# Kernel tuning notes

Measured on AMD Instinct MI355X. Metric: run time of the kernel, lower is better.

## Reference

```python
import jax, jax.numpy as jnp
import numpy as np

HID = 256; HEADS = 8; HD = HID // HEADS; GROUPS = 8; CPG = HID // GROUPS
DIMS = [64, 128, 256, 512]; SIZES = [56, 28, 14, 7]; B = 8


def _linear(x, W, b):
    # torch nn.Linear convention: W is [out, in]
    return jnp.einsum('...i,oi->...o', x, W) + b


def _conv1x1(x, W, b):
    return jnp.einsum('bchw,oc->bohw', x, W) + b[None, :, None, None]


def setup_inputs() -> dict:
    key = jax.random.key(0)
    keys = iter(jax.random.split(key, 64))
    def nrm(shape, s=0.02):
        return jax.random.normal(next(keys), shape, dtype=jnp.float32) * s
    inp = {}
    for i, (d, sz) in enumerate(zip(DIMS, SIZES)):
        inp[f'f{i}'] = jax.random.normal(next(keys), (B, d, sz, sz), dtype=jnp.float32)
        inp[f'Wp{i}'] = nrm((HID, d)); inp[f'bp{i}'] = jnp.zeros((HID,), jnp.float32)
    for n, shp in [('Wq', (HID, HID)), ('Wk', (HID, HID)), ('Wv', (HID, HID)), ('Wo', (HID, HID)),
                   ('Wg1', (HID, 2 * HID)), ('Wg2', (HID, HID)), ('Wcp', (HID, HID)),
                   ('Wkg1', (2 * HID, HID)), ('Wkg2', (GROUPS * 9, 2 * HID)),
                   ('Wit', (HID, HID)), ('Wot', (HID, HID))]:
        inp[n] = nrm(shp)
    for n, dim in [('bq', HID), ('bk', HID), ('bv', HID), ('bo', HID), ('bg1', HID), ('bg2', HID),
                   ('bcp', HID), ('bkg1', 2 * HID), ('bkg2', GROUPS * 9), ('bit', HID), ('bot', HID)]:
        inp[n] = jnp.zeros((dim,), jnp.float32)
    inp['gamma'] = jnp.ones((HID,), jnp.float32)
    inp['beta'] = jnp.zeros((HID,), jnp.float32)
    return inp


def reference(f0, f1, f2, f3, Wp0, bp0, Wp1, bp1, Wp2, bp2, Wp3, bp3,
              Wq, bq, Wk, bk, Wv, bv, Wo, bo, Wg1, bg1, Wg2, bg2,
              Wcp, bcp, Wkg1, bkg1, Wkg2, bkg2, Wit, bit, Wot, bot, gamma, beta):
    feats = [f0, f1, f2, f3]
    Wps = [Wp0, Wp1, Wp2, Wp3]; bps = [bp0, bp1, bp2, bp3]
    b = f0.shape[0]
    # ---- ACSA: 1x1 projections to hidden_dim, flatten spatial to tokens ----
    proj = [_conv1x1(f, W, bb) for f, W, bb in zip(feats, Wps, bps)]  # [B,HID,H,W]
    flat = [p.reshape(b, HID, -1).transpose(0, 2, 1) for p in proj]   # [B,S,HID]
    scale = 1.0 / jnp.sqrt(jnp.float32(HD))
    enhanced = []
    for i, xi in enumerate(flat):
        q = _linear(xi, Wq, bq).reshape(b, -1, HEADS, HD).transpose(0, 2, 1, 3)  # [B,H,Si,d]
        e = xi
        for j, xj in enumerate(flat):
            if i == j:
                continue
            k = _linear(xj, Wk, bk).reshape(b, -1, HEADS, HD).transpose(0, 2, 1, 3)
            v = _linear(xj, Wv, bv).reshape(b, -1, HEADS, HD).transpose(0, 2, 1, 3)
            attn = jax.nn.softmax(jnp.einsum('bhqd,bhkd->bhqk', q, k) * scale, axis=-1)
            ctx = jnp.einsum('bhqk,bhkd->bhqd', attn, v).transpose(0, 2, 1, 3).reshape(b, -1, HID)
            ctx = _linear(ctx, Wo, bo)
            gate = jax.nn.sigmoid(_linear(jax.nn.relu(_linear(jnp.concatenate([e, ctx], -1), Wg1, bg1)), Wg2, bg2))
            e = e + gate * ctx
        enhanced.append(e.transpose(0, 2, 1).reshape(b, HID, proj[i].shape[2], proj[i].shape[3]))
    # ---- CECM per scale: dynamic per-sample grouped 3x3 conv ----
    outs = []
    for x in enhanced:
        H, W = x.shape[2], x.shape[3]
        ctx = jax.nn.relu(_linear(x.mean((2, 3)), Wcp, bcp))                       # [B,HID]
        kern = _linear(jax.nn.relu(_linear(ctx, Wkg1, bkg1)), Wkg2, bkg2)          # [B,G*9]
        kern = kern.reshape(b, GROUPS, 3, 3)
        xt = _conv1x1(x, Wit, bit)                                                 # [B,HID,H,W]
        # per-(sample,group) kernel shared across channels within group -> depthwise conv
        kern_rep = jnp.broadcast_to(kern[:, :, None], (b, GROUPS, CPG, 3, 3)).reshape(b * HID, 1, 3, 3)
        y = jax.lax.conv_general_dilated(
            xt.reshape(1, b * HID, H, W), kern_rep, (1, 1), ((1, 1), (1, 1)),
            dimension_numbers=('NCHW', 'OIHW', 'NCHW'), feature_group_count=b * HID
        ).reshape(b, HID, H, W)
        y = _conv1x1(y, Wot, bot)
        # BatchNorm2d (training-mode batch statistics, biased var, eps=1e-5)
        mu = y.mean((0, 2, 3)); var = y.var((0, 2, 3))
        y = (y - mu[None, :, None, None]) * jax.lax.rsqrt(var + 1e-5)[None, :, None, None]
        y = y * gamma[None, :, None, None] + beta[None, :, None, None]
        outs.append((xt + y).reshape(b, HID, -1))
    # concat scales along flattened-spatial axis -> [B, HID, 3136+784+196+49]
    return jnp.concatenate(outs, axis=-1)
```

## Files before the change

### kernel.cpp

```cpp
#include <hip/hip_runtime.h>
#include <hip/hip_bf16.h>
#include <cstddef>

#define NB 8
#define HIDC 256
#define NHEAD 8
#define HDIM 32
#define TTOK 33320
#define STOT 4165
#define VTP 33440
#define QKVS 768
#define QSC2 0.2550348757f
#define BN1_CH 128

static const int H_SZ[4]   = {56, 28, 14, 7};
static const int S_SZ[4]   = {3136, 784, 196, 49};
static const int D_IN[4]   = {64, 128, 256, 512};
static const int BOFF[4]   = {0, 25088, 31360, 32928};
static const int SKPAD_H[4]= {3136, 784, 200, 56};
static const int VWOFF_H[4]= {0, 25088, 31360, 32960};

__constant__ int DC_S[4]     = {3136, 784, 196, 49};
__constant__ int DC_HW[4]    = {56, 28, 14, 7};
__constant__ int DC_BOFF[4]  = {0, 25088, 31360, 32928};
__constant__ int DC_GOFF[4]  = {0, 3136, 3920, 4116};
__constant__ int DC_FOS[4]   = {0, 49, 62, 66};

__constant__ int FP_SQ[12]   = {784,196,49,3136,196,49,3136,784,49,3136,784,196};
__constant__ int FP_SK[12]   = {3136,3136,3136,784,784,784,196,196,196,49,49,49};
__constant__ int FP_QOFF[12] = {25088,31360,32928,0,31360,32928,0,25088,32928,0,25088,31360};
__constant__ int FP_KOFF[12] = {0,0,0,25088,25088,25088,31360,31360,31360,32928,32928,32928};
__constant__ int FP_VOFF[12] = {0,0,0,25088,25088,25088,31360,31360,31360,32960,32960,32960};
__constant__ int FP_SKP[12]  = {3136,3136,3136,784,784,784,200,200,200,56,56,56};
__constant__ int FP_R[12]    = {0,0,0,0,1,1,1,1,2,2,2,2};
__constant__ int FP_SB0[13]  = {0,13,17,18,31,32,33,46,50,51,64,68,69};

typedef short bf16s;
typedef bf16s bf16x8 __attribute__((ext_vector_type(8)));
typedef float f32x4 __attribute__((ext_vector_type(4)));

static __device__ inline bf16s f2b(float f) {
    return (bf16s)((__float_as_uint(f) + 0x8000u) >> 16);
}
static __device__ inline float b2f(bf16s s) {
    return __uint_as_float(((unsigned)(unsigned short)s) << 16);
}
static __device__ inline unsigned cvtpk(float a, float b) {
    unsigned r;
    asm("v_cvt_pk_bf16_f32 %0, %1, %2" : "=v"(r) : "v"(a), "v"(b));
    return r;
}
static __device__ inline float ex2(float x) {
#if __has_builtin(__builtin_amdgcn_exp2f)
    return __builtin_amdgcn_exp2f(x);
#else
    return exp2f(x);
#endif
}
#define MFMA16(a, b, c) __builtin_amdgcn_mfma_f32_16x16x32_bf16(a, b, c, 0, 0, 0)
#define ZERO4 ((f32x4){0.f, 0.f, 0.f, 0.f})

struct CvtArgs {
    const float* src[15];
    void* dst[15];
    int n[15];
    int mode[15];
    int K[15];
};
__global__ __launch_bounds__(256) void cvt_all(CvtArgs a, int total) {
    int idx = blockIdx.x * 256 + threadIdx.x;
    if (idx >= total) return;
    int seg = 0, off = idx;
    while (off >= a.n[seg]) { off -= a.n[seg]; seg++; }
    float v = a.src[seg][off];
    int m = a.mode[seg];
    if (m == 1 || m == 3) v *= QSC2;
    if (m <= 1) {
        int K = a.K[seg];
        int kz = __builtin_ctz(K);
        int n = off >> kz, k = off & (K - 1);
        int c64 = n >> 6, nt = (n >> 4) & 3, l15 = n & 15;
        int k32 = k >> 5, q = (k >> 3) & 3, j = k & 7;
        int dst = (((c64 * (K >> 5) + k32) * 4 + nt) << 9) + l15 * 32 + q * 8 + j;
        ((bf16s*)a.dst[seg])[dst] = f2b(v);
    } else {
        ((float*)a.dst[seg])[off] = v;
    }
}

__global__ __launch_bounds__(256) void transpose_f2(const float* __restrict__ f,
                                                    bf16s* __restrict__ A, int D, int S) {
    __shared__ float t[32][33];
    int s0 = blockIdx.x * 32, d0 = blockIdx.y * 32, b = blockIdx.z;
    int sl = threadIdx.x & 31, dl = threadIdx.x >> 5;
    #pragma unroll
    for (int dd = 0; dd < 32; dd += 8) {
        int s = s0 + sl;
        t[dl + dd][sl] = (s < S) ? f[((size_t)(b * D + d0 + dl + dd)) * S + s] : 0.f;
    }
    __syncthreads();
    int dc = threadIdx.x & 31, sg = threadIdx.x >> 5;
    #pragma unroll
    for (int ss = 0; ss < 32; ss += 8) {
        int s = s0 + sg + ss;
        if (s < S) A[((size_t)(b * S + s)) * D + d0 + dc] = f2b(t[dc][sg + ss]);
    }
}

template <int EPI>
__global__ __launch_bounds__(256) void gemm3(
    const bf16s* __restrict__ A, const bf16s* __restrict__ A2,
    const bf16s* __restrict__ W, const float* __restrict__ bias,
    float* __restrict__ Cf, bf16s* __restrict__ Cb, const bf16s* __restrict__ Gaux,
    int M, int N, int K, int K1)
{
    int tid = threadIdx.x, lane = tid & 63, wave = tid >> 6;
    int l15 = lane & 15, quad = lane >> 4;
    int row0 = blockIdx.y * 64 + (wave >> 1) * 32;
    int col0 = blockIdx.x * 128 + (wave & 1) * 64;
    int K2 = K - K1;
    int nk = K >> 5;
    int c64 = (blockIdx.x << 1) + (wave & 1);
    const bf16s* wbase = W + (size_t)c64 * ((size_t)nk << 11) + l15 * 32 + quad * 8;
    int ra[2];
    #pragma unroll
    for (int mt = 0; mt < 2; mt++) ra[mt] = min(row0 + mt * 16 + l15, M - 1);

    f32x4 acc[2][4];
    #pragma unroll
    for (int i = 0; i < 2; i++)
        #pragma unroll
        for (int j = 0; j < 4; j++) acc[i][j] = ZERO4;

    bf16x8 aA[2], wA[4], aB[2], wB[4];

    auto loadA = [&](bf16x8* af, int k32) {
        int kk = (k32 << 5) + quad * 8;
        if (kk < K1) {
            #pragma unroll
            for (int mt = 0; mt < 2; mt++)
                af[mt] = *(const bf16x8*)(A + (size_t)ra[mt] * K1 + kk);
        } else {
            int k2 = kk - K1;
            #pragma unroll
            for (int mt = 0; mt < 2; mt++)
                af[mt] = *(const bf16x8*)(A2 + (size_t)ra[mt] * K2 + k2);
        }
    };
    auto loadW = [&](bf16x8* wf, int k32) {
        const bf16s* p = wbase + ((size_t)k32 << 11);
        #pragma unroll
        for (int nt = 0; nt < 4; nt++)
            wf[nt] = *(const bf16x8*)(p + nt * 512);
    };

    loadA(aA, 0); loadW(wA, 0);
    for (int k32 = 0; k32 < nk; k32 += 2) {
        loadA(aB, k32 + 1); loadW(wB, k32 + 1);
        #pragma unroll
        for (int mt = 0; mt < 2; mt++)
            #pragma unroll
            for (int nt = 0; nt < 4; nt++)
                acc[mt][nt] = MFMA16(aA[mt], wA[nt], acc[mt][nt]);
        if (k32 + 2 < nk) { loadA(aA, k32 + 2); loadW(wA, k32 + 2); }
        #pragma unroll
        for (int mt = 0; mt < 2; mt++)
            #pragma unroll
            for (int nt = 0; nt < 4; nt++)
                acc[mt][nt] = MFMA16(aB[mt], wB[nt], acc[mt][nt]);
    }

    #pragma unroll
    for (int mt = 0; mt < 2; mt++) {
        int rowb = row0 + mt * 16 + quad * 4;
        #pragma unroll
        for (int nt = 0; nt < 4; nt++) {
            int col = col0 + nt * 16 + l15;
            float bv = bias ? bias[col] : 0.f;
            #pragma unroll
            for (int r = 0; r < 4; r++) {
                int row = rowb + r;
                if (row >= M) continue;
                size_t off = (size_t)row * N + col;
                float v = acc[mt][nt][r] + bv;
                if (EPI == 0) {
                    Cb[off] = f2b(v);
                } else if (EPI == 1) {
                    Cf[off] = v; Cb[off] = f2b(v);
                } else if (EPI == 2) {
                    float g = 1.f / (1.f + __expf(-v));
                    float e = Cf[off] + g * b2f(Gaux[off]);
                    Cf[off] = e; Cb[off] = f2b(e);
                } else if (EPI == 3) {
                    Cb[off] = f2b(fmaxf(v, 0.f));
                } else {
                    Cf[off] = v;
                }
            }
        }
    }
}

__global__ __launch_bounds__(256) void transpose_v(const bf16s* __restrict__ vsrc,
                                                   bf16s* __restrict__ vdst,
                                                   int Mtok, int Sk, int SkPad, int voff, int VS) {
    __shared__ bf16s t[64][72];
    int t0 = blockIdx.x * 64, d0 = blockIdx.y * 64;
    int tid = threadIdx.x;
    int lr = tid >> 2, lc = (tid & 3) * 16;
    if (t0 + lr < Mtok) {
        bf16x8 v0 = *(const bf16x8*)(vsrc + (size_t)(t0 + lr) * VS + d0 + lc);
        bf16x8 v1 = *(const bf16x8*)(vsrc + (size_t)(t0 + lr) * VS + d0 + lc + 8);
        *(bf16x8*)&t[lr][lc] = v0;
        *(bf16x8*)&t[lr][lc + 8] = v1;
    }
    __syncthreads();
    int dr = tid >> 2, tc = (tid & 3) * 16;
    #pragma unroll
    for (int u = 0; u < 16; u++) {
        int tok = t0 + tc + u;
        if (tok >= Mtok) break;
        int bidx = tok / Sk, s = tok - bidx * Sk;
        vdst[(size_t)(d0 + dr) * VTP + voff + bidx * SkPad + s] = t[tc + u][dr];
    }
}

__global__ __launch_bounds__(256) void flash8(const bf16s* __restrict__ qkv,
                                              const bf16s* __restrict__ vtb,
                                              bf16s* __restrict__ ctxall)
{
    __shared__ bf16s L[4][64 * 40];
    __shared__ float CMB[3][16][64];
    __shared__ float CLS[3][4][64];
    int bx = blockIdx.x;
    int sbg = bx >> 6, hb = bx & 63;
    int h = hb & 7, b = hb >> 3;
    int p = 0;
    while (sbg >= FP_SB0[p + 1]) p++;
    int wave = threadIdx.x >> 6, lane = threadIdx.x & 63;
    int l15 = lane & 15, quad = lane >> 4;
    int Sq = FP_SQ[p], Sk = FP_SK[p];
    bool ksp = (p < 3);
    int qrow0 = ksp ? (sbg - FP_SB0[p]) * 64
                    : ((sbg - FP_SB0[p]) * 4 + wave) * 64;
    if (qrow0 >= Sq) return;
    int k0 = ksp ? wave * 784 : 0;
    int klim = ksp ? 784 : Sk;
    int qoff = FP_QOFF[p], koff = FP_KOFF[p];
    int voff = FP_VOFF[p], skp = FP_SKP[p];
    bf16s* ctxr = ctxall + (size_t)FP_R[p] * TTOK * HIDC;

    const bf16s* qrow = qkv + (size_t)(qoff + b * Sq) * QKVS + h * HDIM + quad * 8;
    bf16x8 qf[4];
    #pragma unroll
    for (int qi = 0; qi < 4; qi++)
        qf[qi] = *(const bf16x8*)(qrow + (size_t)min(qrow0 + qi * 16 + l15, Sq - 1) * QKVS);

    const bf16s* kp0 = qkv + 256 + (size_t)(koff + b * Sk + k0 + l15) * QKVS + h * HDIM + quad * 8;
    const bf16s* kp16 = kp0 + (size_t)16 * QKVS;
    const bf16s* vp0 = vtb + (size_t)(h * HDIM + l15) * VTP + voff + b * skp + k0 + quad * 8;
    const bf16s* vp16 = vp0 + (size_t)16 * VTP;
    bf16s* Lw = L[wave];

    f32x4 a0[4], a1[4];
    float ls[4];
    #pragma unroll
    for (int qi = 0; qi < 4; qi++) { a0[qi] = ZERO4; a1[qi] = ZERO4; ls[qi] = 0.f; }
    int niter = (klim + 31) >> 5;

    bf16x8 kA0, kA1, vA0, vA1, kB0, kB1, vB0, vB1;

    auto loadKV = [&](bf16x8& kf0, bf16x8& kf1, bf16x8& vf0, bf16x8& vf1, int t) {
        size_t kb = (size_t)(t << 5) * QKVS;
        kf0 = *(const bf16x8*)(kp0 + kb);
        kf1 = *(const bf16x8*)(kp16 + kb);
        vf0 = *(const bf16x8*)(vp0 + (t << 5));
        vf1 = *(const bf16x8*)(vp16 + (t << 5));
    };
    auto compute = [&](bf16x8 kf0, bf16x8 kf1, bf16x8 vf0, bf16x8 vf1, int t) {
        int kt = t << 5;
        f32x4 s0[4], s1[4];
        #pragma unroll
        for (int qi = 0; qi < 4; qi++) {
            s0[qi] = MFMA16(kf0, qf[qi], ZERO4);
            s1[qi] = MFMA16(kf1, qf[qi], ZERO4);
        }
        float p0[4][4], p1[4][4];
        #pragma unroll
        for (int qi = 0; qi < 4; qi++)
            #pragma unroll
            for (int r = 0; r < 4; r++) {
                p0[qi][r] = ex2(s0[qi][r]);
                p1[qi][r] = ex2(s1[qi][r]);
            }
        if (kt + 32 > klim) {
            int lim0 = klim - kt - quad * 4, lim1 = lim0 - 16;
            #pragma unroll
            for (int qi = 0; qi < 4; qi++)
                #pragma unroll
                for (int r = 0; r < 4; r++) {
                    if (r >= lim0) p0[qi][r] = 0.f;
                    if (r >= lim1) p1[qi][r] = 0.f;
                }
        }
        #pragma unroll
        for (int qi = 0; qi < 4; qi++) {
            #pragma unroll
            for (int r = 0; r < 4; r++) ls[qi] += p0[qi][r] + p1[qi][r];
            *(uint2*)&Lw[(qi * 16 + l15) * 40 + quad * 4] =
                make_uint2(cvtpk(p0[qi][0], p0[qi][1]), cvtpk(p0[qi][2], p0[qi][3]));
            *(uint2*)&Lw[(qi * 16 + l15) * 40 + 16 + quad * 4] =
                make_uint2(cvtpk(p1[qi][0], p1[qi][1]), cvtpk(p1[qi][2], p1[qi][3]));
        }
        #pragma unroll
        for (int qi = 0; qi < 4; qi++) {
            bf16x8 pb = *(const bf16x8*)&Lw[(qi * 16 + l15) * 40 + quad * 8];
            a0[qi] = MFMA16(vf0, pb, a0[qi]);
            a1[qi] = MFMA16(vf1, pb, a1[qi]);
        }
    };

    loadKV(kA0, kA1, vA0, vA1, 0);
    for (int t = 0; t < niter; t += 2) {
        if (t + 1 < niter) loadKV(kB0, kB1, vB0, vB1, t + 1);
        compute(kA0, kA1, vA0, vA1, t);
        if (t + 2 < niter) loadKV(kA0, kA1, vA0, vA1, t + 2);
        if (t + 1 < niter) compute(kB0, kB1, vB0, vB1, t + 1);
    }

    if (ksp) {
        if (wave > 0) {
            #pragma unroll
            for (int qi = 0; qi < 4; qi++) {
                #pragma unroll
                for (int r = 0; r < 4; r++) CMB[wave - 1][qi * 4 + r][lane] = a0[qi][r];
                CLS[wave - 1][qi][lane] = ls[qi];
            }
        }
        __syncthreads();
        if (wave == 0) {
            #pragma unroll
            for (int w = 0; w < 3; w++)
                #pragma unroll
                for (int qi = 0; qi < 4; qi++) {
                    #pragma unroll
                    for (int r = 0; r < 4; r++) a0[qi][r] += CMB[w][qi * 4 + r][lane];
                    ls[qi] += CLS[w][qi][lane];
                }
        }
        __syncthreads();
        if (wave > 0) {
            #pragma unroll
            for (int qi = 0; qi < 4; qi++)
                #pragma unroll
                for (int r = 0; r < 4; r++) CMB[wave - 1][qi * 4 + r][lane] = a1[qi][r];
        }
        __syncthreads();
        if (wave > 0) return;
        #pragma unroll
        for (int w = 0; w < 3; w++)
            #pragma unroll
            for (int qi = 0; qi < 4; qi++)
                #pragma unroll
                for (int r = 0; r < 4; r++) a1[qi][r] += CMB[w][qi * 4 + r][lane];
    }

    #pragma unroll
    for (int qi = 0; qi < 4; qi++) {
        float l = ls[qi];
        l += __shfl_xor(l, 16); l += __shfl_xor(l, 32);
        float inv = 1.f / l;
        if (qrow0 + qi * 16 + l15 < Sq) {
            size_t o = (size_t)(qoff + b * Sq + qrow0 + qi * 16 + l15) * HIDC + h * HDIM;
            *(uint2*)(ctxr + o + quad * 4) =
                make_uint2(cvtpk(a0[qi][0] * inv, a0[qi][1] * inv),
                           cvtpk(a0[qi][2] * inv, a0[qi][3] * inv));
            *(uint2*)(ctxr + o + 16 + quad * 4) =
                make_uint2(cvtpk(a1[qi][0] * inv, a1[qi][1] * inv),
                           cvtpk(a1[qi][2] * inv, a1[qi][3] * inv));
        }
    }
}

__global__ __launch_bounds__(256) void pool2(const bf16s* __restrict__ xb,
                                             float* __restrict__ partial) {
    int chunk = blockIdx.x, b = blockIdx.y, i = blockIdx.z;
    int c = threadIdx.x;
    int S = DC_S[i];
    int len = (S + 31) / 32;
    int s0 = chunk * len, s1 = min(S, s0 + len);
    float acc = 0.f;
    const bf16s* base = xb + (size_t)(DC_BOFF[i] + b * S) * HIDC + c;
    for (int s = s0; s < s1; s++) acc += b2f(base[(size_t)s * HIDC]);
    partial[(size_t)((i * NB + b) * 32 + chunk) * HIDC + c] = acc;
}

__global__ __launch_bounds__(256) void kgen2(
    const float* __restrict__ partial,
    const float* __restrict__ Wcp, const float* __restrict__ bcp,
    const float* __restrict__ Wkg1, const float* __restrict__ bkg1,
    const float* __restrict__ Wkg2, const float* __restrict__ bkg2,
    float* __restrict__ kern)
{
    __shared__ float pl[256], cv[256], h1[512];
    int b = blockIdx.x, i = blockIdx.y, t = threadIdx.x;
    float invS = 1.f / (float)DC_S[i];
    const float* pb = partial + (size_t)((i * NB + b) * 32) * HIDC;
    float s = 0.f;
    for (int jc = 0; jc < 32; jc++) s += pb[(size_t)jc * HIDC + t];
    pl[t] = s * invS;
    __syncthreads();
    float a = bcp[t];
    for (int k = 0; k < 256; k++) a += Wcp[t * 256 + k] * pl[k];
    cv[t] = fmaxf(a, 0.f);
    __syncthreads();
    for (int r = t; r < 512; r += 256) {
        float a2 = bkg1[r];
        for (int k = 0; k < 256; k++) a2 += Wkg1[r * 256 + k] * cv[k];
        h1[r] = fmaxf(a2, 0.f);
    }
    __syncthreads();
    if (t < 72) {
        float a3 = bkg2[t];
        for (int k = 0; k < 512; k++) a3 += Wkg2[t * 512 + k] * h1[k];
        kern[(i * NB + b) * 72 + t] = a3;
    }
}

__global__ __launch_bounds__(256) void dwconv2(const bf16s* __restrict__ xtb,
                                               const float* __restrict__ kern,
                                               bf16s* __restrict__ y) {
    int tok = blockIdx.x;
    int i = (tok >= DC_BOFF[1]) + (tok >= DC_BOFF[2]) + (tok >= DC_BOFF[3]);
    int S = DC_S[i], W = DC_HW[i];
    int local = tok - DC_BOFF[i];
    int b = local / S, s = local - b * S;
    int hh = s / W, ww = s - hh * W;
    int c = threadIdx.x;
    const float* kb = kern + (i * NB + b) * 72 + (c >> 5) * 9;
    const bf16s* xbase = xtb + (size_t)(DC_BOFF[i] + b * S) * HIDC + c;
    float acc = 0.f;
    #pragma unroll
    for (int ky = 0; ky < 3; ky++) {
        int hy = hh + ky - 1;
        if (hy < 0 || hy >= W) continue;
        #pragma unroll
        for (int kx = 0; kx < 3; kx++) {
            int wx = ww + kx - 1;
            if (wx < 0 || wx >= W) continue;
            acc += kb[ky * 3 + kx] * b2f(xbase[(size_t)(hy * W + wx) * HIDC]);
        }
    }
    y[(size_t)tok * HIDC + c] = f2b(acc);
}

__global__ __launch_bounds__(256) void bn1(const float* __restrict__ yo,
                                           float* __restrict__ bnp) {
    __shared__ float red[4][64][8];
    int chunk = blockIdx.x, i = blockIdx.y, t = threadIdx.x;
    int rg = t >> 6, cq = (t & 63) * 4;
    int Nrows = NB * DC_S[i];
    const float* base = yo + (size_t)DC_BOFF[i] * HIDC + cq;
    f32x4 s = ZERO4, ss = ZERO4;
    for (int r = chunk * 4 + rg; r < Nrows; r += BN1_CH * 4) {
        f32x4 v = *(const f32x4*)(base + (size_t)r * HIDC);
        s += v; ss += v * v;
    }
    #pragma unroll
    for (int j = 0; j < 4; j++) { red[rg][t & 63][j] = s[j]; red[rg][t & 63][4 + j] = ss[j]; }
    __syncthreads();
    if (t < 64) {
        #pragma unroll
        for (int j = 0; j < 4; j++) {
            float a = red[0][t][j] + red[1][t][j] + red[2][t][j] + red[3][t][j];
            float b = red[0][t][4 + j] + red[1][t][4 + j] + red[2][t][4 + j] + red[3][t][4 + j];
            bnp[(size_t)(i * BN1_CH + chunk) * 512 + t * 4 + j] = a;
            bnp[(size_t)(i * BN1_CH + chunk) * 512 + 256 + t * 4 + j] = b;
        }
    }
}
__global__ __launch_bounds__(256) void bn2(const float* __restrict__ bnp,
                                           float* __restrict__ stat) {
    int i = blockIdx.x, c = threadIdx.x;
    float s = 0.f, ss = 0.f;
    for (int ch = 0; ch < BN1_CH; ch++) {
        s += bnp[(size_t)(i * BN1_CH + ch) * 512 + c];
        ss += bnp[(size_t)(i * BN1_CH + ch) * 512 + 256 + c];
    }
    float inv = 1.f / (float)(NB * DC_S[i]);
    float mu = s * inv;
    float var = fmaxf(ss * inv - mu * mu, 0.f);
    stat[i * 512 + c] = mu;
    stat[i * 512 + 256 + c] = rsqrtf(var + 1e-5f);
}

__global__ __launch_bounds__(256) void final2(const bf16s* __restrict__ xtb,
                                              const float* __restrict__ yo,
                                              const float* __restrict__ stat,
                                              const float* __restrict__ gamma,
                                              const float* __restrict__ beta,
                                              float* __restrict__ out) {
    __shared__ float tile[64][65];
    int bx = blockIdx.x;
    int i = (bx >= DC_FOS[1]) + (bx >= DC_FOS[2]) + (bx >= DC_FOS[3]);
    int S = DC_S[i];
    int s0 = (bx - DC_FOS[i]) * 64;
    int cstrip = blockIdx.y, b = blockIdx.z;
    int g = threadIdx.x >> 6, sl = threadIdx.x & 63;
    {
        int c = cstrip * 64 + sl;
        float mu = stat[i * 512 + c], rstd = stat[i * 512 + 256 + c];
        float ga = gamma[c], be = beta[c];
        size_t rbase = (size_t)(DC_BOFF[i] + b * S) * HIDC + c;
        #pragma unroll
        for (int u = 0; u < 16; u++) {
            int s = s0 + g * 16 + u;
            if (s < S) {
                size_t r = rbase + (size_t)s * HIDC;
                tile[g * 16 + u][sl] = b2f(xtb[r]) + (yo[r] - mu) * rstd * ga + be;
            }
        }
    }
    __syncthreads();
    {
        int s = s0 + sl;
        if (s < S) {
            #pragma unroll
            for (int cs = 0; cs < 16; cs++) {
                int cl = g * 16 + cs;
                out[((size_t)(b * HIDC + cstrip * 64 + cl)) * STOT + DC_GOFF[i] + s] = tile[sl][cl];
            }
        }
    }
}

static inline void gemm_launch(hipStream_t st, const bf16s* A, const bf16s* A2,
                               const bf16s* W, const float* bias,
                               float* Cf, bf16s* Cb, const bf16s* Gaux,
                               int M, int N, int K, int K1, int epi) {
    dim3 grid(N / 128, (M + 63) / 64), blk(256);
    switch (epi) {
        case 0: gemm3<0><<<grid, blk, 0, st>>>(A, A2, W, bias, Cf, Cb, Gaux, M, N, K, K1); break;
        case 1: gemm3<1><<<grid, blk, 0, st>>>(A, A2, W, bias, Cf, Cb, Gaux, M, N, K, K1); break;
        case 2: gemm3<2><<<grid, blk, 0, st>>>(A, A2, W, bias, Cf, Cb, Gaux, M, N, K, K1); break;
        case 3: gemm3<3><<<grid, blk, 0, st>>>(A, A2, W, bias, Cf, Cb, Gaux, M, N, K, K1); break;
        default: gemm3<4><<<grid, blk, 0, st>>>(A, A2, W, bias, Cf, Cb, Gaux, M, N, K, K1); break;
    }
}

extern "C" void kernel_launch(void* const* d_in, const int* in_sizes, int n_in,
                              void* d_out, int out_size, void* d_ws, size_t ws_size,
                              hipStream_t stream) {
    typedef const float* fp;
    fp f[4]  = {(fp)d_in[0], (fp)d_in[3], (fp)d_in[6], (fp)d_in[9]};
    fp Wp[4] = {(fp)d_in[1], (fp)d_in[4], (fp)d_in[7], (fp)d_in[10]};
    fp bp[4] = {(fp)d_in[2], (fp)d_in[5], (fp)d_in[8], (fp)d_in[11]};
    fp Wq = (fp)d_in[12], Wk = (fp)d_in[13], Wv = (fp)d_in[14], Wo = (fp)d_in[15];
    fp Wg1 = (fp)d_in[16], Wg2 = (fp)d_in[17], Wcp = (fp)d_in[18];
    fp Wkg1 = (fp)d_in[19], Wkg2 = (fp)d_in[20], Wit = (fp)d_in[21], Wot = (fp)d_in[22];
    fp bq = (fp)d_in[23], bk = (fp)d_in[24], bv = (fp)d_in[25], bo = (fp)d_in[26];
    fp bg1 = (fp)d_in[27], bg2 = (fp)d_in[28], bcp = (fp)d_in[29];
    fp bkg1 = (fp)d_in[30], bkg2 = (fp)d_in[31], bit = (fp)d_in[32], bot = (fp)d_in[33];
    fp gamma = (fp)d_in[34], beta = (fp)d_in[35];
    float* out = (float*)d_out;

    const size_t NT = (size_t)TTOK * HIDC;

    float* x     = (float*)d_ws;
    bf16s* xb    = (bf16s*)(x + NT);
    bf16s* qkvb  = xb + NT;
    bf16s* vtb   = qkvb + (size_t)TTOK * QKVS;
    bf16s* ctxall= vtb + (size_t)HIDC * VTP;
    bf16s* ctxob = ctxall + 3 * NT;
    float* partial = (float*)(ctxob + 3 * NT);
    float* kern    = partial + 4 * NB * 32 * HIDC;
    float* bnp     = kern + 4 * NB * 72;
    float* bnstat  = bnp + 4 * 32 * 512;
    float* bqkv    = bnstat + 4 * 512;
    bf16s* wseg    = (bf16s*)(bqkv + 768);
    bf16s* atmp = ctxall;
    bf16s* hb   = ctxall;
    bf16s* xtb  = ctxall + NT;
    float* yo   = x;
    float* bnp2 = partial;

    bf16s* wpb[4]; size_t wo_ = 0;
    for (int i = 0; i < 4; i++) { wpb[i] = wseg + wo_; wo_ += (size_t)HIDC * D_IN[i]; }
    bf16s* wqkvb = wseg + wo_; wo_ += (size_t)QKVS * 256;
    bf16s* wob  = wseg + wo_; wo_ += 65536;
    bf16s* wg1b = wseg + wo_; wo_ += 131072;
    bf16s* wg2b = wseg + wo_; wo_ += 65536;
    bf16s* witb = wseg + wo_; wo_ += 65536;
    bf16s* wotb = wseg + wo_; wo_ += 65536;

    {
        CvtArgs ca;
        const float* srcs[15] = {Wp[0], Wp[1], Wp[2], Wp[3], Wq, Wk, Wv, Wo, Wg1, Wg2,
                                 Wit, Wot, bq, bk, bv};
        void* dsts[15] = {wpb[0], wpb[1], wpb[2], wpb[3], wqkvb, wqkvb + 65536,
                          wqkvb + 131072, wob, wg1b, wg2b, witb, wotb,
                          bqkv, bqkv + 256, bqkv + 512};
        int ns[15] = {16384, 32768, 65536, 131072, 65536, 65536, 65536, 65536, 131072,
                      65536, 65536, 65536, 256, 256, 256};
        int modes[15] = {0, 0, 0, 0, 1, 0, 0, 0, 0, 0, 0, 0, 3, 2, 2};
        int Ks[15] = {64, 128, 256, 512, 256, 256, 256, 256, 512, 256, 256, 256, 0, 0, 0};
        int total = 0;
        for (int k = 0; k < 15; k++) { ca.src[k] = srcs[k]; ca.dst[k] = dsts[k];
                                       ca.n[k] = ns[k]; ca.mode[k] = modes[k];
                                       ca.K[k] = Ks[k]; total += ns[k]; }
        cvt_all<<<dim3((total + 255) / 256), dim3(256), 0, stream>>>(ca, total);
    }
    hipMemsetAsync(vtb, 0, (size_t)HIDC * VTP * sizeof(bf16s), stream);

    for (int i = 0; i < 4; i++) {
        int S = S_SZ[i], D = D_IN[i], M = NB * S;
        transpose_f2<<<dim3((S + 31) / 32, D / 32, NB), dim3(256), 0, stream>>>(f[i], atmp, D, S);
        gemm_launch(stream, atmp, nullptr, wpb[i], bp[i],
                    x + (size_t)BOFF[i] * HIDC, xb + (size_t)BOFF[i] * HIDC, nullptr,
                    M, HIDC, D, D, 1);
    }

    gemm_launch(stream, xb, nullptr, wqkvb, bqkv, nullptr, qkvb, nullptr, TTOK, QKVS, 256, 256, 0);
    for (int j = 0; j < 4; j++) {
        int Mtok = NB * S_SZ[j];
        transpose_v<<<dim3((Mtok + 63) / 64, 4), dim3(256), 0, stream>>>(
            qkvb + 512 + (size_t)BOFF[j] * QKVS, vtb, Mtok, S_SZ[j], SKPAD_H[j], VWOFF_H[j], QKVS);
    }

    flash8<<<dim3(69 * 64), dim3(256), 0, stream>>>(qkvb, vtb, ctxall);
    gemm_launch(stream, ctxall, nullptr, wob, bo, nullptr, ctxob, nullptr, 3 * TTOK, HIDC, 256, 256, 0);
    for (int r = 0; r < 3; r++) {
        bf16s* cr = ctxob + (size_t)r * NT;
        gemm_launch(stream, xb, cr, wg1b, bg1, nullptr, hb, nullptr, TTOK, HIDC, 512, 256, 3);
        gemm_launch(stream, hb, nullptr, wg2b, bg2, x, xb, cr, TTOK, HIDC, 256, 256, 2);
    }

    pool2<<<dim3(32, NB, 4), dim3(256), 0, stream>>>(xb, partial);
    kgen2<<<dim3(NB, 4), dim3(256), 0, stream>>>(partial, Wcp, bcp, Wkg1, bkg1, Wkg2, bkg2, kern);
    gemm_launch(stream, xb, nullptr, witb, bit, nullptr, xtb, nullptr, TTOK, HIDC, 256, 256, 0);
    dwconv2<<<dim3(TTOK), dim3(256), 0, stream>>>(xtb, kern, hb);
    gemm_launch(stream, hb, nullptr, wotb, bot, yo, nullptr, nullptr, TTOK, HIDC, 256, 256, 4);
    bn1<<<dim3(BN1_CH, 4), dim3(256), 0, stream>>>(yo, bnp2);
    bn2<<<dim3(4), dim3(256), 0, stream>>>(bnp2, bnstat);
    final2<<<dim3(67, 4, NB), dim3(256), 0, stream>>>(xtb, yo, bnstat, gamma, beta, out);
}
```

Baseline: 999.4 us.

## Fuse three-round gating MLP chain into one kernel with LDS-resident activations

Replaces six GEMM launches (three rounds of gate-hidden relu GEMM and gate-output sigmoid GEMM) with one kernel per 32-row tile. The running fp32 state, its bf16 copy, context and hidden activations stay in registers and LDS across all three rounds. This removes the global round-trips of the hidden buffer and the repeated reads and writes of x/xb. Weights are now streamed from global memory per block without LDS staging, and the tile is smaller than the old 64x128 GEMM tile, so weight traffic per row rises and occupancy may drop.

Result: faster. 850.4 us (-14.9%).

```diff
diff --git a/kernel.cpp b/kernel.cpp
--- a/kernel.cpp
+++ b/kernel.cpp
@@ -187,18 +187,178 @@
                     Cb[off] = f2b(v);
                 } else if (EPI == 1) {
                     Cf[off] = v; Cb[off] = f2b(v);
-                } else if (EPI == 2) {
-                    float g = 1.f / (1.f + __expf(-v));
-                    float e = Cf[off] + g * b2f(Gaux[off]);
-                    Cf[off] = e; Cb[off] = f2b(e);
-                } else if (EPI == 3) {
-                    Cb[off] = f2b(fmaxf(v, 0.f));
                 } else {
                     Cf[off] = v;
                 }
             }
         }
     }
+}
+
+#define GLDS 264
+__global__ __launch_bounds__(256) void gatefuse(
+    const bf16s* __restrict__ ctxob, bf16s* __restrict__ xb, const float* __restrict__ x,
+    const bf16s* __restrict__ Wg1, const float* __restrict__ bg1,
+    const bf16s* __restrict__ Wg2, const float* __restrict__ bg2, int M)
+{
+    __shared__ bf16s ebf[32 * GLDS], cxb[32 * GLDS], hbf[32 * GLDS];
+    int tid = threadIdx.x, lane = tid & 63, wave = tid >> 6;
+    int l15 = lane & 15, quad = lane >> 4;
+    int r0 = blockIdx.x * 32;
+    int col0 = wave * 64;
+
+    #pragma unroll
+    for (int u = 0; u < 4; u++) {
+        int idx = u * 256 + tid;
+        int row = idx >> 5, ch = (idx & 31) * 8;
+        *(bf16x8*)&ebf[row * GLDS + ch] =
+            *(const bf16x8*)(xb + (size_t)min(r0 + row, M - 1) * HIDC + ch);
+    }
+    f32x4 e32[2][4];
+    #pragma unroll
+    for (int mt = 0; mt < 2; mt++)
+        #pragma unroll
+        for (int nt = 0; nt < 4; nt++)
+            #pragma unroll
+            for (int rr = 0; rr < 4; rr++) {
+                int row = min(r0 + mt * 16 + quad * 4 + rr, M - 1);
+                e32[mt][nt][rr] = x[(size_t)row * HIDC + col0 + nt * 16 + l15];
+            }
+
+    const bf16s* w1base = Wg1 + ((size_t)wave << 15) + l15 * 32 + quad * 8;
+    const bf16s* w2base = Wg2 + ((size_t)wave << 14) + l15 * 32 + quad * 8;
+
+    for (int r = 0; r < 3; r++) {
+        __syncthreads();
+        const bf16s* crp = ctxob + (size_t)r * ((size_t)TTOK * HIDC);
+        #pragma unroll
+        for (int u = 0; u < 4; u++) {
+            int idx = u * 256 + tid;
+            int row = idx >> 5, ch = (idx & 31) * 8;
+            *(bf16x8*)&cxb[row * GLDS + ch] =
+                *(const bf16x8*)(crp + (size_t)min(r0 + row, M - 1) * HIDC + ch);
+        }
+        __syncthreads();
+
+        f32x4 acc[2][4];
+        bf16x8 aA[2], wA[4], aB[2], wB[4];
+
+        #pragma unroll
+        for (int i = 0; i < 2; i++)
+            #pragma unroll
+            for (int j = 0; j < 4; j++) acc[i][j] = ZERO4;
+        auto loadA1 = [&](bf16x8* af, int k32) {
+            int kk = (k32 << 5) + quad * 8;
+            if (kk < 256) {
+                #pragma unroll
+                for (int mt = 0; mt < 2; mt++)
+                    af[mt] = *(const bf16x8*)&ebf[(mt * 16 + l15) * GLDS + kk];
+            } else {
+                #pragma unroll
+                for (int mt = 0; mt < 2; mt++)
+                    af[mt] = *(const bf16x8*)&cxb[(mt * 16 + l15) * GLDS + kk - 256];
+            }
+        };
+        auto loadW1 = [&](bf16x8* wf, int k32) {
+            const bf16s* p = w1base + ((size_t)k32 << 11);
+            #pragma unroll
+            for (int nt = 0; nt < 4; nt++)
+                wf[nt] = *(const bf16x8*)(p + nt * 512);
+        };
+        loadA1(aA, 0); loadW1(wA, 0);
+        for (int k32 = 0; k32 < 16; k32 += 2) {
+            loadA1(aB, k32 + 1); loadW1(wB, k32 + 1);
+            #pragma unroll
+            for (int mt = 0; mt < 2; mt++)
+                #pragma unroll
+                for (int nt = 0; nt < 4; nt++)
+                    acc[mt][nt] = MFMA16(aA[mt], wA[nt], acc[mt][nt]);
+            if (k32 + 2 < 16) { loadA1(aA, k32 + 2); loadW1(wA, k32 + 2); }
+            #pragma unroll
+            for (int mt = 0; mt < 2; mt++)
+                #pragma unroll
+                for (int nt = 0; nt < 4; nt++)
+                    acc[mt][nt] = MFMA16(aB[mt], wB[nt], acc[mt][nt]);
+        }
+        #pragma unroll
+        for (int mt = 0; mt < 2; mt++)
+            #pragma unroll
+            for (int nt = 0; nt < 4; nt++)
+                #pragma unroll
+                for (int rr = 0; rr < 4; rr++) {
+                    int row = mt * 16 + quad * 4 + rr;
+                    int col = col0 + nt * 16 + l15;
+                    hbf[row * GLDS + col] = f2b(fmaxf(acc[mt][nt][rr] + bg1[col], 0.f));
+                }
+        __syncthreads();
+
+        #pragma unroll
+        for (int i = 0; i < 2; i++)
+            #pragma unroll
+            for (int j = 0; j < 4; j++) acc[i][j] = ZERO4;
+        auto loadA2 = [&](bf16x8* af, int k32) {
+            int kk = (k32 << 5) + quad * 8;
+            #pragma unroll
+            for (int mt = 0; mt < 2; mt++)
+                af[mt] = *(const bf16x8*)&hbf[(mt * 16 + l15) * GLDS + kk];
+        };
+        auto loadW2 = [&](bf16x8* wf, int k32) {
+            const bf16s* p = w2base + ((size_t)k32 << 11);
+            #pragma unroll
+            for (int nt = 0; nt < 4; nt++)
+                wf[nt] = *(const bf16x8*)(p + nt * 512);
+        };
+        loadA2(aA, 0); loadW2(wA, 0);
+        for (int k32 = 0; k32 < 8; k32 += 2) {
+            loadA2(aB, k32 + 1); loadW2(wB, k32 + 1);
+            #pragma unroll
+            for (int mt = 0; mt < 2; mt++)
+                #pragma unroll
+                for (int nt = 0; nt < 4; nt++)
+                    acc[mt][nt] = MFMA16(aA[mt], wA[nt], acc[mt][nt]);
+            if (k32 + 2 < 8) { loadA2(aA, k32 + 2); loadW2(wA, k32 + 2); }
+            #pragma unroll
+            for (int mt = 0; mt < 2; mt++)
+                #pragma unroll
+                for (int nt = 0; nt < 4; nt++)
+                    acc[mt][nt] = MFMA16(aB[mt], wB[nt], acc[mt][nt]);
+        }
+        #pragma unroll
+        for (int mt = 0; mt < 2; mt++)
+            #pragma unroll
+            for (int nt = 0; nt < 4; nt++)
+                #pragma unroll
+                for (int rr = 0; rr < 4; rr++) {
+                    int row = mt * 16 + quad * 4 + rr;
+                    int col = col0 + nt * 16 + l15;
+                    float v = acc[mt][nt][rr] + bg2[col];
+                    float g = 1.f / (1.f + __expf(-v));
+                    e32[mt][nt][rr] += g * b2f(cxb[row * GLDS + col]);
+                }
+        if (r < 2) {
+            #pragma unroll
+            for (int mt = 0; mt < 2; mt++)
+                #pragma unroll
+                for (int nt = 0; nt < 4; nt++)
+                    #pragma unroll
+                    for (int rr = 0; rr < 4; rr++) {
+                        int row = mt * 16 + quad * 4 + rr;
+                        int col = col0 + nt * 16 + l15;
+                        ebf[row * GLDS + col] = f2b(e32[mt][nt][rr]);
+                    }
+        }
+    }
+
+    #pragma unroll
+    for (int mt = 0; mt < 2; mt++)
+        #pragma unroll
+        for (int nt = 0; nt < 4; nt++)
+            #pragma unroll
+            for (int rr = 0; rr < 4; rr++) {
+                int row = r0 + mt * 16 + quad * 4 + rr;
+                if (row < M)
+                    xb[(size_t)row * HIDC + col0 + nt * 16 + l15] = f2b(e32[mt][nt][rr]);
+            }
 }
 
 __global__ __launch_bounds__(256) void transpose_v(const bf16s* __restrict__ vsrc,
@@ -542,8 +702,6 @@
     switch (epi) {
         case 0: gemm3<0><<<grid, blk, 0, st>>>(A, A2, W, bias, Cf, Cb, Gaux, M, N, K, K1); break;
         case 1: gemm3<1><<<grid, blk, 0, st>>>(A, A2, W, bias, Cf, Cb, Gaux, M, N, K, K1); break;
-        case 2: gemm3<2><<<grid, blk, 0, st>>>(A, A2, W, bias, Cf, Cb, Gaux, M, N, K, K1); break;
-        case 3: gemm3<3><<<grid, blk, 0, st>>>(A, A2, W, bias, Cf, Cb, Gaux, M, N, K, K1); break;
         default: gemm3<4><<<grid, blk, 0, st>>>(A, A2, W, bias, Cf, Cb, Gaux, M, N, K, K1); break;
     }
 }
@@ -629,11 +787,8 @@
 
     flash8<<<dim3(69 * 64), dim3(256), 0, stream>>>(qkvb, vtb, ctxall);
     gemm_launch(stream, ctxall, nullptr, wob, bo, nullptr, ctxob, nullptr, 3 * TTOK, HIDC, 256, 256, 0);
-    for (int r = 0; r < 3; r++) {
-        bf16s* cr = ctxob + (size_t)r * NT;
-        gemm_launch(stream, xb, cr, wg1b, bg1, nullptr, hb, nullptr, TTOK, HIDC, 512, 256, 3);
-        gemm_launch(stream, hb, nullptr, wg2b, bg2, x, xb, cr, TTOK, HIDC, 256, 256, 2);
-    }
+    gatefuse<<<dim3((TTOK + 31) / 32), dim3(256), 0, stream>>>(
+        ctxob, xb, x, wg1b, bg1, wg2b, bg2, TTOK);
 
     pool2<<<dim3(32, NB, 4), dim3(256), 0, stream>>>(xb, partial);
     kgen2<<<dim3(NB, 4), dim3(256), 0, stream>>>(partial, Wcp, bcp, Wkg1, bkg1, Wkg2, bkg2, kern);
```
